# Optimization experiments

Hardware: AMD Instinct MI355X
Metric: run time of the kernel (lower is better)

Reference implementation:

```python
import jax, jax.numpy as jnp
import numpy as np
import itertools
jax.config.update("jax_enable_x64", True)

ND, NQ, B = 4, 3, 256          # ndrives, nqubits, batch_size
D = 2 ** NQ                     # Hilbert-space dim = 8


def _pauli_basis(nq):
    I = np.eye(2, dtype=np.complex128)
    X = np.array([[0, 1], [1, 0]], dtype=np.complex128)
    Y = np.array([[0, -1j], [1j, 0]], dtype=np.complex128)
    Z = np.array([[1, 0], [0, -1]], dtype=np.complex128)
    mats = []
    for combo in itertools.product([I, X, Y, Z], repeat=nq):
        m = np.array([[1.0 + 0j]], dtype=np.complex128)
        for s in combo:
            m = np.kron(m, s)
        mats.append(m)
    return np.stack(mats)  # [4**nq, 2**nq, 2**nq], Hermitian


def setup_inputs() -> dict:
    key = jax.random.key(0)
    k1, k2, k3 = jax.random.split(key, 3)
    paulies = jnp.asarray(_pauli_basis(NQ))          # [64, 8, 8] complex128
    L = paulies.shape[0]
    x = jax.random.normal(k1, (B, ND), dtype=jnp.float64)
    # keras 'normal' initializer ~ stddev 0.05
    kernel = 0.05 * jax.random.normal(k2, (ND, L), dtype=jnp.float64)
    bias = 0.05 * jax.random.normal(k3, (L,), dtype=jnp.float64)
    return {"x": x, "kernel": kernel, "bias": bias, "paulies": paulies}


def _probs(pw_i, paulies):
    # pw_i: [L] real pauli weights for one sample
    H = jnp.tensordot(pw_i.astype(jnp.complex128), paulies, axes=[[0], [0]])  # [D, D]
    e, v = jnp.linalg.eigh(H)                      # Hermitian eigendecomp
    expe = jnp.exp(-1j * e)                        # [D]
    # amp_j = sum_s conj(v)[0,s] * exp(-i e_s) * v[j,s]  (evolution of |0>)
    amp = jnp.einsum('s,js->j', jnp.conj(v[0, :]) * expe, v)  # [D]
    return amp.real ** 2 + amp.imag ** 2           # P, [D] float64


def reference(x, kernel, bias, paulies):
    pw = x @ kernel + bias                         # [B, L]
    f = lambda p: _probs(p, paulies)
    P = jax.vmap(f)(pw)                            # [B, D]
    # per-sample Jacobian dP/d(pauli_weights): [B, D, L]
    g = jax.vmap(jax.jacrev(f))(pw)
    oneoverp = 1.0 / P                             # [B, D]
    # chain rule: pw = x @ kernel + bias  =>  dP/dkernel[i,p,j,k] = x[i,j] * g[i,p,k]
    p_k = jnp.einsum('ij,ipk->ipjk', x, g)         # [B, D, ND, L]
    I_k = jnp.einsum('ipjk,iplm,ip->ijklm', p_k, p_k, oneoverp)  # [B, ND, L, ND, L]
    I_b = jnp.einsum('ipj,ipk,ip->ijk', g, g, oneoverp)          # [B, L, L]
    return (I_k, I_b)
```

## Files before the change

kernel.cpp:

```cpp
#include <hip/hip_runtime.h>
#include <math.h>

__device__ __forceinline__ double rdin(const void* p, int idx, bool isdbl) {
  return isdbl ? ((const double*)p)[idx] : (double)((const float*)p)[idx];
}

__device__ __forceinline__ bool detect_dbl(const void* xv) {
  const float* xq = (const float*)xv;
  bool isdbl = false;
  for (int j = 0; j < 64; ++j) {
    float a = fabsf(xq[j]);
    if (!(a < 1e6f)) isdbl = true;
  }
  return isdbl;
}

__global__ __launch_bounds__(64) void fi_phase1(
    const void* __restrict__ xv,
    const void* __restrict__ kv,
    const void* __restrict__ bv,
    float* __restrict__ out, int Bn)
{
  const int i = blockIdx.x;
  const int t = threadIdx.x;

  __shared__ float pw[64];
  __shared__ float Hre[8][8], Him[8][8];
  __shared__ float Vre[8][8], Vim[8][8];
  __shared__ float Fre[8][8], Fim[8][8];
  __shared__ float Gre[8][8], Gim[8][8];
  __shared__ float ampre[8], ampim[8], invPs[8], ev[8];
  __shared__ __align__(16) float hk[64][8];

  const bool isdbl = detect_dbl(xv);

  {
    float acc = (float)rdin(bv, t, isdbl);
    #pragma unroll
    for (int j = 0; j < 4; ++j)
      acc += (float)rdin(xv, i*4 + j, isdbl) * (float)rdin(kv, j*64 + t, isdbl);
    pw[t] = acc;
  }
  __syncthreads();

  {
    int r = t >> 3, c = t & 7;
    int m = r ^ c;
    float hre = 0.0f, him = 0.0f;
    for (int u = 0; u < 8; ++u) {
      int k = 0;
      float pr = 1.0f, pim = 0.0f;
      #pragma unroll
      for (int q = 0; q < 3; ++q) {
        int bit = 2 - q;
        int f  = (m >> bit) & 1;
        int ch = (u >> bit) & 1;
        int rb = (r >> bit) & 1;
        int d  = f ? (ch ? 2 : 1) : (ch ? 3 : 0);
        k = (k << 2) | d;
        if (d == 2) {
          float nr = rb ? -pim : pim;
          float ni = rb ?  pr  : -pr;
          pr = nr; pim = ni;
        } else if (d == 3 && rb) { pr = -pr; pim = -pim; }
      }
      float w = pw[k];
      hre += w * pr; him += w * pim;
    }
    Hre[r][c] = hre; Him[r][c] = him;
    Vre[r][c] = (r == c) ? 1.0f : 0.0f;
    Vim[r][c] = 0.0f;
  }
  __syncthreads();

  const int tl = t & 31;
  const int pp = tl >> 3, j = tl & 7;
  #pragma unroll
  for (int sweep = 0; sweep < 4; ++sweep) {
    #pragma unroll
    for (int round = 0; round < 7; ++round) {
      int p, q;
      if (pp == 0) { p = 7; q = round; }
      else {
        p = round + pp;     if (p >= 7) p -= 7;
        q = round + 7 - pp; if (q >= 7) q -= 7;
      }
      float cc = 1.0f, sg = 0.0f, wr = 1.0f, wi = 0.0f;
      {
        float a = Hre[p][p], b = Hre[q][q];
        float zr = Hre[p][q], zi = Him[p][q];
        float r2 = zr*zr + zi*zi;
        if (r2 > 1e-24f) {
          float rr = sqrtf(r2);
          wr = zr / rr; wi = zi / rr;
          float th = (b - a) / (2.0f * rr);
          float tt = ((th >= 0.0f) ? 1.0f : -1.0f) / (fabsf(th) + sqrtf(1.0f + th*th));
          cc = 1.0f / sqrtf(1.0f + tt*tt);
          sg = tt * cc;
        }
      }
      float e0r, e0i, e1r, e1i;
      if (t < 32) { e0r = Hre[j][p]; e0i = Him[j][p]; e1r = Hre[j][q]; e1i = Him[j][q]; }
      else        { e0r = Vre[j][p]; e0i = Vim[j][p]; e1r = Vre[j][q]; e1i = Vim[j][q]; }
      __syncthreads();
      if (t < 32) {
        Hre[j][p] = cc*e0r - sg*(wr*e1r + wi*e1i);
        Him[j][p] = cc*e0i - sg*(wr*e1i - wi*e1r);
        Hre[j][q] = sg*(wr*e0r - wi*e0i) + cc*e1r;
        Him[j][q] = sg*(wr*e0i + wi*e0r) + cc*e1i;
      } else {
        Vre[j][p] = cc*e0r - sg*(wr*e1r + wi*e1i);
        Vim[j][p] = cc*e0i - sg*(wr*e1i - wi*e1r);
        Vre[j][q] = sg*(wr*e0r - wi*e0i) + cc*e1r;
        Vim[j][q] = sg*(wr*e0i + wi*e0r) + cc*e1i;
      }
      __syncthreads();
      if (t < 32) {
        float rpr = Hre[p][j], rpi = Him[p][j];
        float rqr = Hre[q][j], rqi = Him[q][j];
        Hre[p][j] = cc*rpr - sg*(wr*rqr - wi*rqi);
        Him[p][j] = cc*rpi - sg*(wr*rqi + wi*rqr);
        Hre[q][j] = sg*(wr*rpr + wi*rpi) + cc*rqr;
        Him[q][j] = sg*(wr*rpi - wi*rpr) + cc*rqi;
      }
      __syncthreads();
    }
  }

  if (t < 8) ev[t] = Hre[t][t];
  __syncthreads();

  {
    int s = t >> 3, u = t & 7;
    float dm = 0.5f * (ev[s] - ev[u]);
    float av = 0.5f * (ev[s] + ev[u]);
    float sc = (fabsf(dm) < 1e-3f) ? (1.0f - dm*dm*(1.0f/6.0f)) : (__sinf(dm)/dm);
    Fre[s][u] =  __cosf(av) * sc;
    Fim[s][u] = -__sinf(av) * sc;
  }
  if (t < 8) {
    float are = 0.0f, aim = 0.0f;
    #pragma unroll
    for (int s = 0; s < 8; ++s) {
      float ce = __cosf(ev[s]), se = -__sinf(ev[s]);
      float c0r = Vre[0][s], c0i = -Vim[0][s];
      float wr2 = c0r*ce - c0i*se;
      float wi2 = c0r*se + c0i*ce;
      float vjr = Vre[t][s], vji = Vim[t][s];
      are += vjr*wr2 - vji*wi2;
      aim += vjr*wi2 + vji*wr2;
    }
    ampre[t] = are; ampim[t] = aim;
    float P = are*are + aim*aim;
    invPs[t] = 1.0f / fmaxf(P, 1e-30f);
  }
  __syncthreads();

  {
    int s = t >> 3, rho = t & 7;
    float gr = 0.0f, gi = 0.0f;
    #pragma unroll
    for (int u = 0; u < 8; ++u) {
      float c0r = Vre[0][u], c0i = -Vim[0][u];
      float fr = Fre[s][u], fi = Fim[s][u];
      float fcr = fr*c0r - fi*c0i;
      float fci = fr*c0i + fi*c0r;
      float vr = Vre[rho][u], vi = Vim[rho][u];
      gr += vr*fcr - vi*fci;
      gi += vr*fci + vi*fcr;
    }
    Gre[s][rho] = gr; Gim[s][rho] = gi;
  }
  __syncthreads();

  float gcol[8];
  {
    const int k = t;
    const int d0 = (k >> 4) & 3, d1 = (k >> 2) & 3, d2 = k & 3;
    const int m = ((((d0 == 1) | (d0 == 2)) ? 1 : 0) << 2)
                | ((((d1 == 1) | (d1 == 2)) ? 1 : 0) << 1)
                |  (((d2 == 1) | (d2 == 2)) ? 1 : 0);
    float yre[8], yim[8];
    #pragma unroll
    for (int s = 0; s < 8; ++s) { yre[s] = 0.0f; yim[s] = 0.0f; }
    #pragma unroll
    for (int r = 0; r < 8; ++r) {
      float pr = 1.0f, pim = 0.0f;
      const int dd0[3] = {d0, d1, d2};
      #pragma unroll
      for (int q = 0; q < 3; ++q) {
        int rb = (r >> (2 - q)) & 1;
        int d = dd0[q];
        if (d == 2) {
          float nr = rb ? -pim : pim;
          float ni = rb ?  pr  : -pr;
          pr = nr; pim = ni;
        } else if (d == 3 && rb) { pr = -pr; pim = -pim; }
      }
      int rm = r ^ m;
      #pragma unroll
      for (int s = 0; s < 8; ++s) {
        float vr = Vre[r][s], vi = -Vim[r][s];
        float gr2 = Gre[s][rm], gi2 = Gim[s][rm];
        float ar = pr*gr2 - pim*gi2;
        float ai = pr*gi2 + pim*gr2;
        yre[s] += vr*ar - vi*ai;
        yim[s] += vr*ai + vi*ar;
      }
    }
    #pragma unroll
    for (int p = 0; p < 8; ++p) {
      float dr = 0.0f, di = 0.0f;
      #pragma unroll
      for (int s = 0; s < 8; ++s) {
        float ysr =  yim[s], ysi = -yre[s];
        float vr = Vre[p][s], vi = Vim[p][s];
        dr += vr*ysr - vi*ysi;
        di += vr*ysi + vi*ysr;
      }
      float gg = 2.0f * (ampre[p]*dr + ampim[p]*di);
      gcol[p] = gg;
      hk[k][p] = gg * invPs[p];
    }
  }
  __syncthreads();

  {
    float* ob = out + (size_t)Bn * 65536 + (size_t)i * 4096 + (size_t)t * 64;
    #pragma unroll
    for (int m4 = 0; m4 < 16; ++m4) {
      float4 vv;
      #pragma unroll
      for (int l = 0; l < 4; ++l) {
        int m = m4*4 + l;
        const float4 ha = *(const float4*)&hk[m][0];
        const float4 hb = *(const float4*)&hk[m][4];
        float acc = gcol[0]*ha.x + gcol[1]*ha.y + gcol[2]*ha.z + gcol[3]*ha.w
                  + gcol[4]*hb.x + gcol[5]*hb.y + gcol[6]*hb.z + gcol[7]*hb.w;
        (&vv.x)[l] = acc;
      }
      *(float4*)(ob + m4*4) = vv;
    }
  }
}

__global__ __launch_bounds__(256) void fi_phase2(
    const void* __restrict__ xv,
    float* __restrict__ out, int Bn)
{
  const int bx = blockIdx.x;
  const int i  = bx >> 4;
  const int blk = bx & 15;
  const int t = threadIdx.x;

  __shared__ __align__(16) float Ms[16][68];

  const bool isdbl = detect_dbl(xv);

  const int rg = t >> 4;
  const int q4 = (t & 15) << 2;

  const float* Mg = out + (size_t)Bn * 65536 + (size_t)i * 4096;
  *(float4*)&Ms[rg][q4] =
      *(const float4*)(Mg + (size_t)(((blk & 3) << 4) + rg) * 64 + q4);

  const int j = blk >> 2;
  float xjf = (float)rdin(xv, i*4 + j, isdbl);
  float xx[4];
  #pragma unroll
  for (int l = 0; l < 4; ++l)
    xx[l] = xjf * (float)rdin(xv, i*4 + l, isdbl);

  __syncthreads();

  float* ok = out + (size_t)i * 65536 + (size_t)blk * 4096;
  #pragma unroll
  for (int it = 0; it < 4; ++it) {
    int local = it*16 + rg;
    int kk = local >> 2;
    int l  = local & 3;
    const float4 mv = *(const float4*)&Ms[kk][q4];
    float s = xx[l];
    *(float4*)(ok + (size_t)local * 64 + q4) =
        make_float4(s*mv.x, s*mv.y, s*mv.z, s*mv.w);
  }
}

extern "C" void kernel_launch(void* const* d_in, const int* in_sizes, int n_in,
                              void* d_out, int out_size, void* d_ws, size_t ws_size,
                              hipStream_t stream) {
  (void)n_in; (void)d_ws; (void)ws_size; (void)out_size;
  int Bn = in_sizes[0] / 4;
  fi_phase1<<<Bn, 64, 0, stream>>>(d_in[0], d_in[1], d_in[2], (float*)d_out, Bn);
  fi_phase2<<<Bn * 16, 256, 0, stream>>>(d_in[0], (float*)d_out, Bn);
}
```

Before: 111.8 us.

## Fuse both phases into one kernel, recomputing eigendecomposition per output block

Merges the two kernels into one launch of Bn*16 blocks of 64 threads. Each block redoes the per-sample Hamiltonian eigendecomposition and gradient, then builds its own 16-row slice of the bias Fisher matrix in shared memory and writes the scaled kernel-Fisher block directly. Only block 0 writes I_b. This removes the second launch and the global-memory round trip through the I_b output, at the cost of 16x redundant eigensolver work per sample and fewer threads per output block.

```diff
diff --git a/kernel.cpp b/kernel.cpp
--- a/kernel.cpp
+++ b/kernel.cpp
@@ -15,22 +15,28 @@
   return isdbl;
 }
 
-__global__ __launch_bounds__(64) void fi_phase1(
+__global__ __launch_bounds__(64, 4) void fi_fused(
     const void* __restrict__ xv,
     const void* __restrict__ kv,
     const void* __restrict__ bv,
     float* __restrict__ out, int Bn)
 {
-  const int i = blockIdx.x;
-  const int t = threadIdx.x;
+  const int bx  = blockIdx.x;
+  const int i   = bx >> 4;
+  const int blk = bx & 15;
+  const int t   = threadIdx.x;
 
   __shared__ float pw[64];
   __shared__ float Hre[8][8], Him[8][8];
   __shared__ float Vre[8][8], Vim[8][8];
-  __shared__ float Fre[8][8], Fim[8][8];
-  __shared__ float Gre[8][8], Gim[8][8];
   __shared__ float ampre[8], ampim[8], invPs[8], ev[8];
-  __shared__ __align__(16) float hk[64][8];
+  __shared__ __align__(16) float gk[64][8], hk[64][8];
+  __shared__ __align__(16) float scratch[1024];
+  float (*Fre)[8] = (float(*)[8])(scratch);
+  float (*Fim)[8] = (float(*)[8])(scratch + 64);
+  float (*Gre)[8] = (float(*)[8])(scratch + 128);
+  float (*Gim)[8] = (float(*)[8])(scratch + 192);
+  float (*Ms)[64] = (float(*)[64])(scratch);
 
   const bool isdbl = detect_dbl(xv);
 
@@ -220,12 +226,13 @@
       }
       float gg = 2.0f * (ampre[p]*dr + ampim[p]*di);
       gcol[p] = gg;
+      gk[k][p] = gg;
       hk[k][p] = gg * invPs[p];
     }
   }
   __syncthreads();
 
-  {
+  if (blk == 0) {
     float* ob = out + (size_t)Bn * 65536 + (size_t)i * 4096 + (size_t)t * 64;
     #pragma unroll
     for (int m4 = 0; m4 < 16; ++m4) {
@@ -235,54 +242,47 @@
         int m = m4*4 + l;
         const float4 ha = *(const float4*)&hk[m][0];
         const float4 hb = *(const float4*)&hk[m][4];
-        float acc = gcol[0]*ha.x + gcol[1]*ha.y + gcol[2]*ha.z + gcol[3]*ha.w
-                  + gcol[4]*hb.x + gcol[5]*hb.y + gcol[6]*hb.z + gcol[7]*hb.w;
-        (&vv.x)[l] = acc;
+        (&vv.x)[l] = gcol[0]*ha.x + gcol[1]*ha.y + gcol[2]*ha.z + gcol[3]*ha.w
+                   + gcol[4]*hb.x + gcol[5]*hb.y + gcol[6]*hb.z + gcol[7]*hb.w;
       }
       *(float4*)(ob + m4*4) = vv;
     }
   }
-}
-
-__global__ __launch_bounds__(256) void fi_phase2(
-    const void* __restrict__ xv,
-    float* __restrict__ out, int Bn)
-{
-  const int bx = blockIdx.x;
-  const int i  = bx >> 4;
-  const int blk = bx & 15;
-  const int t = threadIdx.x;
-
-  __shared__ __align__(16) float Ms[16][68];
-
-  const bool isdbl = detect_dbl(xv);
-
-  const int rg = t >> 4;
-  const int q4 = (t & 15) << 2;
-
-  const float* Mg = out + (size_t)Bn * 65536 + (size_t)i * 4096;
-  *(float4*)&Ms[rg][q4] =
-      *(const float4*)(Mg + (size_t)(((blk & 3) << 4) + rg) * 64 + q4);
-
-  const int j = blk >> 2;
-  float xjf = (float)rdin(xv, i*4 + j, isdbl);
-  float xx[4];
-  #pragma unroll
-  for (int l = 0; l < 4; ++l)
-    xx[l] = xjf * (float)rdin(xv, i*4 + l, isdbl);
-
-  __syncthreads();
-
-  float* ok = out + (size_t)i * 65536 + (size_t)blk * 4096;
-  #pragma unroll
-  for (int it = 0; it < 4; ++it) {
-    int local = it*16 + rg;
-    int kk = local >> 2;
-    int l  = local & 3;
-    const float4 mv = *(const float4*)&Ms[kk][q4];
-    float s = xx[l];
-    *(float4*)(ok + (size_t)local * 64 + q4) =
-        make_float4(s*mv.x, s*mv.y, s*mv.z, s*mv.w);
+
+  {
+    const int kbase = (blk & 3) << 4;
+    const float4 ha = *(const float4*)&hk[t][0];
+    const float4 hb = *(const float4*)&hk[t][4];
+    #pragma unroll
+    for (int kk = 0; kk < 16; ++kk) {
+      const float4 ga = *(const float4*)&gk[kbase + kk][0];
+      const float4 gb = *(const float4*)&gk[kbase + kk][4];
+      Ms[kk][t] = ga.x*ha.x + ga.y*ha.y + ga.z*ha.z + ga.w*ha.w
+                + gb.x*hb.x + gb.y*hb.y + gb.z*hb.z + gb.w*hb.w;
+    }
+  }
+  __syncthreads();
+
+  {
+    float xjf = (float)rdin(xv, i*4 + (blk >> 2), isdbl);
+    float xx[4];
+    #pragma unroll
+    for (int l = 0; l < 4; ++l)
+      xx[l] = xjf * (float)rdin(xv, i*4 + l, isdbl);
+
+    float* ok = out + (size_t)i * 65536 + (size_t)blk * 4096;
+    const int rg = t >> 4;
+    const int q4 = (t & 15) << 2;
+    #pragma unroll
+    for (int it = 0; it < 16; ++it) {
+      int local = it*4 + rg;
+      int kk = local >> 2;
+      int l  = local & 3;
+      const float4 mv = *(const float4*)&Ms[kk][q4];
+      float s = xx[l];
+      *(float4*)(ok + (size_t)local * 64 + q4) =
+          make_float4(s*mv.x, s*mv.y, s*mv.z, s*mv.w);
+    }
   }
 }
 
@@ -291,6 +291,6 @@
                               hipStream_t stream) {
   (void)n_in; (void)d_ws; (void)ws_size; (void)out_size;
   int Bn = in_sizes[0] / 4;
-  fi_phase1<<<Bn, 64, 0, stream>>>(d_in[0], d_in[1], d_in[2], (float*)d_out, Bn);
-  fi_phase2<<<Bn * 16, 256, 0, stream>>>(d_in[0], (float*)d_out, Bn);
-}
+  fi_fused<<<Bn * 16, 64, 0, stream>>>(d_in[0], d_in[1], d_in[2],
+                                       (float*)d_out, Bn);
+}
```

New measurement: 126.3 us. +13.0%, slower.

## Restructure Jacobi eigensolver to one element per thread with double-buffered LDS

Applied to the files above, without the earlier changes.

Reworks the parallel Jacobi eigensolver so each of the 64 threads owns one H and one V element in registers. It applies the row and column rotations in a single step and ping-pongs between two LDS buffers, so each round needs one barrier instead of three. Rotation parameters now use hardware rsq/rcp intrinsics instead of divisions and sqrt. The cost is that both rotation parameters are recomputed redundantly in every thread, and the fast intrinsics carry slightly reduced precision.

```diff
diff --git a/kernel.cpp b/kernel.cpp
--- a/kernel.cpp
+++ b/kernel.cpp
@@ -13,6 +13,27 @@
     if (!(a < 1e6f)) isdbl = true;
   }
   return isdbl;
+}
+
+__device__ __forceinline__ void pairup(int v, int round, int& prt, bool& isp) {
+  if (v == 7) { prt = round; isp = true; return; }
+  int o = v - round; if (o < 0) o += 7;
+  if (o == 0) { prt = 7; isp = false; return; }
+  int pr = round + 7 - o; if (pr >= 7) pr -= 7;
+  prt = pr; isp = (o <= 3);
+}
+
+__device__ __forceinline__ void mkparam(float a, float b, float zr, float zi,
+                                        float& cc, float& sg, float& wr, float& wi) {
+  float r2 = zr*zr + zi*zi;
+  if (r2 > 1e-24f) {
+    float irr = __builtin_amdgcn_rsqf(r2);
+    wr = zr * irr; wi = zi * irr;
+    float th = (b - a) * 0.5f * irr;
+    float tt = copysignf(__builtin_amdgcn_rcpf(fabsf(th) + sqrtf(1.0f + th*th)), th);
+    cc = __builtin_amdgcn_rsqf(1.0f + tt*tt);
+    sg = tt * cc;
+  } else { cc = 1.0f; sg = 0.0f; wr = 1.0f; wi = 0.0f; }
 }
 
 __global__ __launch_bounds__(64) void fi_phase1(
@@ -23,14 +44,13 @@
 {
   const int i = blockIdx.x;
   const int t = threadIdx.x;
-
+  const int r = t >> 3, c = t & 7;
+
+  __shared__ float Sb[2][4][64];
   __shared__ float pw[64];
-  __shared__ float Hre[8][8], Him[8][8];
-  __shared__ float Vre[8][8], Vim[8][8];
-  __shared__ float Fre[8][8], Fim[8][8];
-  __shared__ float Gre[8][8], Gim[8][8];
-  __shared__ float ampre[8], ampim[8], invPs[8], ev[8];
-  __shared__ __align__(16) float hk[64][8];
+  __shared__ float FreS[64], FimS[64], GreS[64], GimS[64];
+  __shared__ float ampre[8], ampim[8], invPs[8], evs[8];
+  __shared__ __align__(16) float gk[64][8], hk[64][8];
 
   const bool isdbl = detect_dbl(xv);
 
@@ -43,8 +63,8 @@
   }
   __syncthreads();
 
-  {
-    int r = t >> 3, c = t & 7;
+  float hr, hi, vr_, vi_;
+  {
     int m = r ^ c;
     float hre = 0.0f, him = 0.0f;
     for (int u = 0; u < 8; ++u) {
@@ -67,86 +87,94 @@
       float w = pw[k];
       hre += w * pr; him += w * pim;
     }
-    Hre[r][c] = hre; Him[r][c] = him;
-    Vre[r][c] = (r == c) ? 1.0f : 0.0f;
-    Vim[r][c] = 0.0f;
-  }
-  __syncthreads();
-
-  const int tl = t & 31;
-  const int pp = tl >> 3, j = tl & 7;
-  #pragma unroll
-  for (int sweep = 0; sweep < 4; ++sweep) {
-    #pragma unroll
-    for (int round = 0; round < 7; ++round) {
-      int p, q;
-      if (pp == 0) { p = 7; q = round; }
-      else {
-        p = round + pp;     if (p >= 7) p -= 7;
-        q = round + 7 - pp; if (q >= 7) q -= 7;
-      }
-      float cc = 1.0f, sg = 0.0f, wr = 1.0f, wi = 0.0f;
-      {
-        float a = Hre[p][p], b = Hre[q][q];
-        float zr = Hre[p][q], zi = Him[p][q];
-        float r2 = zr*zr + zi*zi;
-        if (r2 > 1e-24f) {
-          float rr = sqrtf(r2);
-          wr = zr / rr; wi = zi / rr;
-          float th = (b - a) / (2.0f * rr);
-          float tt = ((th >= 0.0f) ? 1.0f : -1.0f) / (fabsf(th) + sqrtf(1.0f + th*th));
-          cc = 1.0f / sqrtf(1.0f + tt*tt);
-          sg = tt * cc;
-        }
-      }
-      float e0r, e0i, e1r, e1i;
-      if (t < 32) { e0r = Hre[j][p]; e0i = Him[j][p]; e1r = Hre[j][q]; e1i = Him[j][q]; }
-      else        { e0r = Vre[j][p]; e0i = Vim[j][p]; e1r = Vre[j][q]; e1i = Vim[j][q]; }
-      __syncthreads();
-      if (t < 32) {
-        Hre[j][p] = cc*e0r - sg*(wr*e1r + wi*e1i);
-        Him[j][p] = cc*e0i - sg*(wr*e1i - wi*e1r);
-        Hre[j][q] = sg*(wr*e0r - wi*e0i) + cc*e1r;
-        Him[j][q] = sg*(wr*e0i + wi*e0r) + cc*e1i;
-      } else {
-        Vre[j][p] = cc*e0r - sg*(wr*e1r + wi*e1i);
-        Vim[j][p] = cc*e0i - sg*(wr*e1i - wi*e1r);
-        Vre[j][q] = sg*(wr*e0r - wi*e0i) + cc*e1r;
-        Vim[j][q] = sg*(wr*e0i + wi*e0r) + cc*e1i;
-      }
-      __syncthreads();
-      if (t < 32) {
-        float rpr = Hre[p][j], rpi = Him[p][j];
-        float rqr = Hre[q][j], rqi = Him[q][j];
-        Hre[p][j] = cc*rpr - sg*(wr*rqr - wi*rqi);
-        Him[p][j] = cc*rpi - sg*(wr*rqi + wi*rqr);
-        Hre[q][j] = sg*(wr*rpr + wi*rpi) + cc*rqr;
-        Him[q][j] = sg*(wr*rpi - wi*rpr) + cc*rqi;
-      }
-      __syncthreads();
-    }
-  }
-
-  if (t < 8) ev[t] = Hre[t][t];
+    hr = hre; hi = him;
+    vr_ = (r == c) ? 1.0f : 0.0f;
+    vi_ = 0.0f;
+  }
+  Sb[0][0][t] = hr; Sb[0][1][t] = hi;
+  Sb[0][2][t] = vr_; Sb[0][3][t] = vi_;
+  __syncthreads();
+
+  float* curB = &Sb[0][0][0];
+  float* nxtB = &Sb[1][0][0];
+  int round = 0;
+  #pragma unroll 1
+  for (int it = 0; it < 28; ++it) {
+    int rho, gam; bool isPr, isPc;
+    pairup(r, round, rho, isPr);
+    pairup(c, round, gam, isPc);
+    const int pR = isPr ? r : rho, qR = isPr ? rho : r;
+    const int pC = isPc ? c : gam, qC = isPc ? gam : c;
+
+    const float* HreC = curB;
+    const float* HimC = curB + 64;
+    const float* VreC = curB + 128;
+    const float* VimC = curB + 192;
+
+    float aR  = HreC[pR*9],    bR  = HreC[qR*9];
+    float zRr = HreC[pR*8+qR], zRi = HimC[pR*8+qR];
+    float aC  = HreC[pC*9],    bC  = HreC[qC*9];
+    float zCr = HreC[pC*8+qC], zCi = HimC[pC*8+qC];
+    float hpc_r = HreC[rho*8+c],   hpc_i = HimC[rho*8+c];
+    float hrg_r = HreC[r*8+gam],   hrg_i = HimC[r*8+gam];
+    float hpg_r = HreC[rho*8+gam], hpg_i = HimC[rho*8+gam];
+    float vrg_r = VreC[r*8+gam],   vrg_i = VimC[r*8+gam];
+
+    float cR, sR, wRr, wRi; mkparam(aR, bR, zRr, zRi, cR, sR, wRr, wRi);
+    float cC, sC, wCr, wCi; mkparam(aC, bC, zCr, zCi, cC, sC, wCr, wCi);
+
+    float t1r = wRr*hpc_r - wRi*hpc_i, t1i = wRr*hpc_i + wRi*hpc_r;
+    float u1r = wRr*hpc_r + wRi*hpc_i, u1i = wRr*hpc_i - wRi*hpc_r;
+    float Bc_r = isPr ? (cR*hr - sR*t1r) : (cR*hr + sR*u1r);
+    float Bc_i = isPr ? (cR*hi - sR*t1i) : (cR*hi + sR*u1i);
+    float t2r = wRr*hpg_r - wRi*hpg_i, t2i = wRr*hpg_i + wRi*hpg_r;
+    float u2r = wRr*hpg_r + wRi*hpg_i, u2i = wRr*hpg_i - wRi*hpg_r;
+    float Bg_r = isPr ? (cR*hrg_r - sR*t2r) : (cR*hrg_r + sR*u2r);
+    float Bg_i = isPr ? (cR*hrg_i - sR*t2i) : (cR*hrg_i + sR*u2i);
+
+    float t3r = wCr*Bg_r + wCi*Bg_i, t3i = wCr*Bg_i - wCi*Bg_r;
+    float t4r = wCr*Bg_r - wCi*Bg_i, t4i = wCr*Bg_i + wCi*Bg_r;
+    hr = isPc ? (cC*Bc_r - sC*t3r) : (cC*Bc_r + sC*t4r);
+    hi = isPc ? (cC*Bc_i - sC*t3i) : (cC*Bc_i + sC*t4i);
+
+    float t5r = wCr*vrg_r + wCi*vrg_i, t5i = wCr*vrg_i - wCi*vrg_r;
+    float t6r = wCr*vrg_r - wCi*vrg_i, t6i = wCr*vrg_i + wCi*vrg_r;
+    float nvr = isPc ? (cC*vr_ - sC*t5r) : (cC*vr_ + sC*t6r);
+    float nvi = isPc ? (cC*vi_ - sC*t5i) : (cC*vi_ + sC*t6i);
+    vr_ = nvr; vi_ = nvi;
+
+    nxtB[t]       = hr;
+    nxtB[64 + t]  = hi;
+    nxtB[128 + t] = vr_;
+    nxtB[192 + t] = vi_;
+    float* tmp = curB; curB = nxtB; nxtB = tmp;
+    round = (round == 6) ? 0 : round + 1;
+    __syncthreads();
+  }
+
+  const float* VreF = curB + 128;
+  const float* VimF = curB + 192;
+
+  if (r == c) evs[r] = hr;
   __syncthreads();
 
   {
     int s = t >> 3, u = t & 7;
-    float dm = 0.5f * (ev[s] - ev[u]);
-    float av = 0.5f * (ev[s] + ev[u]);
+    float dm = 0.5f * (evs[s] - evs[u]);
+    float av = 0.5f * (evs[s] + evs[u]);
     float sc = (fabsf(dm) < 1e-3f) ? (1.0f - dm*dm*(1.0f/6.0f)) : (__sinf(dm)/dm);
-    Fre[s][u] =  __cosf(av) * sc;
-    Fim[s][u] = -__sinf(av) * sc;
+    FreS[t] =  __cosf(av) * sc;
+    FimS[t] = -__sinf(av) * sc;
   }
   if (t < 8) {
     float are = 0.0f, aim = 0.0f;
     #pragma unroll
     for (int s = 0; s < 8; ++s) {
-      float ce = __cosf(ev[s]), se = -__sinf(ev[s]);
-      float c0r = Vre[0][s], c0i = -Vim[0][s];
+      float ce = __cosf(evs[s]), se = -__sinf(evs[s]);
+      float c0r = VreF[s], c0i = -VimF[s];
       float wr2 = c0r*ce - c0i*se;
       float wi2 = c0r*se + c0i*ce;
-      float vjr = Vre[t][s], vji = Vim[t][s];
+      float vjr = VreF[t*8+s], vji = VimF[t*8+s];
       are += vjr*wr2 - vji*wi2;
       aim += vjr*wi2 + vji*wr2;
     }
@@ -161,15 +189,15 @@
     float gr = 0.0f, gi = 0.0f;
     #pragma unroll
     for (int u = 0; u < 8; ++u) {
-      float c0r = Vre[0][u], c0i = -Vim[0][u];
-      float fr = Fre[s][u], fi = Fim[s][u];
+      float c0r = VreF[u], c0i = -VimF[u];
+      float fr = FreS[s*8+u], fi = FimS[s*8+u];
       float fcr = fr*c0r - fi*c0i;
       float fci = fr*c0i + fi*c0r;
-      float vr = Vre[rho][u], vi = Vim[rho][u];
+      float vr = VreF[rho*8+u], vi = VimF[rho*8+u];
       gr += vr*fcr - vi*fci;
       gi += vr*fci + vi*fcr;
     }
-    Gre[s][rho] = gr; Gim[s][rho] = gi;
+    GreS[t] = gr; GimS[t] = gi;
   }
   __syncthreads();
 
@@ -184,12 +212,12 @@
     #pragma unroll
     for (int s = 0; s < 8; ++s) { yre[s] = 0.0f; yim[s] = 0.0f; }
     #pragma unroll
-    for (int r = 0; r < 8; ++r) {
+    for (int rr = 0; rr < 8; ++rr) {
       float pr = 1.0f, pim = 0.0f;
       const int dd0[3] = {d0, d1, d2};
       #pragma unroll
       for (int q = 0; q < 3; ++q) {
-        int rb = (r >> (2 - q)) & 1;
+        int rb = (rr >> (2 - q)) & 1;
         int d = dd0[q];
         if (d == 2) {
           float nr = rb ? -pim : pim;
@@ -197,11 +225,11 @@
           pr = nr; pim = ni;
         } else if (d == 3 && rb) { pr = -pr; pim = -pim; }
       }
-      int rm = r ^ m;
+      int rm = rr ^ m;
       #pragma unroll
       for (int s = 0; s < 8; ++s) {
-        float vr = Vre[r][s], vi = -Vim[r][s];
-        float gr2 = Gre[s][rm], gi2 = Gim[s][rm];
+        float vr = VreF[rr*8+s], vi = -VimF[rr*8+s];
+        float gr2 = GreS[s*8+rm], gi2 = GimS[s*8+rm];
         float ar = pr*gr2 - pim*gi2;
         float ai = pr*gi2 + pim*gr2;
         yre[s] += vr*ar - vi*ai;
@@ -214,13 +242,14 @@
       #pragma unroll
       for (int s = 0; s < 8; ++s) {
         float ysr =  yim[s], ysi = -yre[s];
-        float vr = Vre[p][s], vi = Vim[p][s];
+        float vr = VreF[p*8+s], vi = VimF[p*8+s];
         dr += vr*ysr - vi*ysi;
         di += vr*ysi + vi*ysr;
       }
       float gg = 2.0f * (ampre[p]*dr + ampim[p]*di);
       gcol[p] = gg;
-      hk[k][p] = gg * invPs[p];
+      gk[t][p] = gg;
+      hk[t][p] = gg * invPs[p];
     }
   }
   __syncthreads();
@@ -235,9 +264,8 @@
         int m = m4*4 + l;
         const float4 ha = *(const float4*)&hk[m][0];
         const float4 hb = *(const float4*)&hk[m][4];
-        float acc = gcol[0]*ha.x + gcol[1]*ha.y + gcol[2]*ha.z + gcol[3]*ha.w
-                  + gcol[4]*hb.x + gcol[5]*hb.y + gcol[6]*hb.z + gcol[7]*hb.w;
-        (&vv.x)[l] = acc;
+        (&vv.x)[l] = gcol[0]*ha.x + gcol[1]*ha.y + gcol[2]*ha.z + gcol[3]*ha.w
+                   + gcol[4]*hb.x + gcol[5]*hb.y + gcol[6]*hb.z + gcol[7]*hb.w;
       }
       *(float4*)(ob + m4*4) = vv;
     }
```

Measured after the change: 114.0 us. +2.0%, slower.
